# Kernel optimization log

Hardware: AMD Instinct MI355X
Metric: run time of the kernel (lower is better)

The kernel has to match this reference:

```python
import jax, jax.numpy as jnp
import numpy as np

N_NODES = 25000
N_EDGES = 400000
N_GRAPHS = 64
F_IN = 128


def setup_inputs() -> dict:
    key = jax.random.key(0)
    ks = jax.random.split(key, 16)
    inp = {}
    inp["x"] = jax.random.normal(ks[0], (N_NODES, F_IN), dtype=jnp.float32)
    inp["edge_index"] = jax.random.randint(ks[1], (2, N_EDGES), 0, N_NODES, dtype=jnp.int64)
    inp["edge_attr"] = jax.random.uniform(ks[2], (N_EDGES,), dtype=jnp.float32)
    inp["batch_ids"] = jnp.sort(jax.random.randint(ks[3], (N_NODES,), 0, N_GRAPHS, dtype=jnp.int64))
    def lin(k, fan_in, fan_out):
        bound = 1.0 / np.sqrt(fan_in)
        return jax.random.uniform(k, (fan_in, fan_out), dtype=jnp.float32, minval=-bound, maxval=bound)
    inp["W1_rel"] = lin(ks[4], F_IN, 512)
    inp["b1"] = jnp.zeros((512,), jnp.float32)
    inp["W1_root"] = lin(ks[5], F_IN, 512)
    inp["W2_rel"] = lin(ks[6], 512, 512)
    inp["b2"] = jnp.zeros((512,), jnp.float32)
    inp["W2_root"] = lin(ks[7], 512, 512)
    inp["Wl1"] = lin(ks[8], 512, 64)
    inp["bl1"] = jnp.zeros((64,), jnp.float32)
    inp["Wl2"] = lin(ks[9], 64, 16)
    inp["bl2"] = jnp.zeros((16,), jnp.float32)
    inp["Wl3"] = lin(ks[10], 16, 1)
    inp["bl3"] = jnp.zeros((1,), jnp.float32)
    return inp


def _graph_conv(h, src, dst, edge_attr, W_rel, b_rel, W_root, n_nodes):
    # PyG GraphConv: lin_rel(scatter_add(w_e * x_src, dst)) + lin_root(x)
    msg = h[src] * edge_attr[:, None]                       # [E, F] gather
    agg = jax.ops.segment_sum(msg, dst, num_segments=n_nodes)  # [N, F] scatter-add
    return agg @ W_rel + b_rel + h @ W_root


def reference(x, edge_index, edge_attr, batch_ids, W1_rel, b1, W1_root,
              W2_rel, b2, W2_root, Wl1, bl1, Wl2, bl2, Wl3, bl3):
    n_nodes = x.shape[0]
    src, dst = edge_index[0], edge_index[1]
    h = jax.nn.relu(_graph_conv(x, src, dst, edge_attr, W1_rel, b1, W1_root, n_nodes))
    h = jax.nn.relu(_graph_conv(h, src, dst, edge_attr, W2_rel, b2, W2_root, n_nodes))
    # global mean pool by graph id
    sums = jax.ops.segment_sum(h, batch_ids, num_segments=N_GRAPHS)  # [G, 512]
    counts = jax.ops.segment_sum(jnp.ones((n_nodes,), h.dtype), batch_ids, num_segments=N_GRAPHS)
    g = sums / jnp.maximum(counts, 1.0)[:, None]
    # dropout is identity in eval mode
    g = jax.nn.relu(g @ Wl1 + bl1)
    g = jax.nn.relu(g @ Wl2 + bl2)
    return g @ Wl3 + bl3  # [G, 1]
```

## Files before the change

kernel.cpp:

```cpp
#include <hip/hip_runtime.h>
#include <hip/hip_bf16.h>
#include <hip/hip_fp16.h>
#include <stdint.h>

#define N_NODESC 25000
#define N_EDGESC 400000
#define N_GRAPHSC 64
#define F_INC 128
#define HIDC 512
#define PSTRIDE 1600000
#define MTILES 196

typedef __attribute__((ext_vector_type(8))) short short8;
typedef __attribute__((ext_vector_type(8))) _Float16 half8;
typedef __attribute__((ext_vector_type(4))) float f32x4;

__device__ __forceinline__ unsigned short f2h(float f) {
  return __half_as_ushort(__float2half_rn(f));
}

__global__ __launch_bounds__(256)
void prep_kernel(const float* __restrict__ x, const int* __restrict__ ei,
                 const float* __restrict__ W1rel, const float* __restrict__ W1root,
                 const float* __restrict__ W2rel, const float* __restrict__ W2root,
                 unsigned short* __restrict__ xp, unsigned short* __restrict__ W1T,
                 unsigned short* __restrict__ W2T, int* __restrict__ deg,
                 float* __restrict__ gsum) {
  int blk = blockIdx.x, t = threadIdx.x;
  if (blk < 1563) {
    int e = blk * 256 + t;
    if (e < N_EDGESC) atomicAdd(&deg[ei[N_EDGESC + e]], 1);
  } else if (blk < 4688) {
    int idx = ((blk - 1563) * 256 + t) * 4;
    int node = idx >> 7;
    int col = idx & 127;
    float4 v = *(const float4*)(x + idx);
    ushort4 o;
    o.x = f2h(v.x); o.y = f2h(v.y); o.z = f2h(v.z); o.w = f2h(v.w);
    *(ushort4*)(xp + (size_t)(col >> 6) * PSTRIDE + (size_t)node * 64 + (col & 63)) = o;
  } else if (blk < 4848) {
    __shared__ float tile[64][65];
    int b2 = blk - 4688;
    const float* src;
    unsigned short* dst;
    int n0, k0, Kout;
    if (b2 < 128) {
      int kt = b2 >> 3, nt = b2 & 7;
      k0 = kt * 64; n0 = nt * 64;
      src = (k0 < 512) ? (W2rel + (size_t)k0 * 512) : (W2root + (size_t)(k0 - 512) * 512);
      dst = W2T; Kout = 1024;
    } else {
      int b = b2 - 128;
      int kt = b >> 3, nt = b & 7;
      k0 = kt * 64; n0 = nt * 64;
      src = (k0 < 128) ? (W1rel + (size_t)k0 * 512) : (W1root + (size_t)(k0 - 128) * 512);
      dst = W1T; Kout = 256;
    }
    int c = t & 63;
    int r4 = t >> 6;
#pragma unroll
    for (int rr = 0; rr < 64; rr += 4) {
      int row = rr + r4;
      tile[c][row] = src[(size_t)row * 512 + n0 + c];
    }
    __syncthreads();
#pragma unroll
    for (int rr = 0; rr < 64; rr += 4) {
      int nrow = rr + r4;
      dst[(size_t)(n0 + nrow) * Kout + k0 + c] = f2h(tile[nrow][c]);
    }
  } else {
    int i = (blk - 4848) * 256 + t;
    if (i < N_GRAPHSC * HIDC) gsum[i] = 0.f;
  }
}

__global__ __launch_bounds__(1024)
void scan_kernel(const int* __restrict__ deg, int* __restrict__ indptr, int* __restrict__ cursor,
                 int* __restrict__ sorted) {
  __shared__ int sums[1024];
  __shared__ int bins[256];
  __shared__ int binptr[256];
  const int t = threadIdx.x;
  const int CH = (N_NODESC + 1023) / 1024;
  const int base = t * CH;
  const unsigned ub = (unsigned)deg[N_NODESC];
  if (t < 256) bins[t] = 0;
  __syncthreads();
  int dl[CH];
  int s = 0;
  for (int i = 0; i < CH; ++i) {
    int idx = base + i;
    int d = (idx < N_NODESC) ? (int)((unsigned)deg[idx] - ub) : -1;
    dl[i] = d;
    if (d >= 0) {
      s += d;
      atomicAdd(&bins[d > 255 ? 255 : d], 1);
    }
  }
  sums[t] = s;
  __syncthreads();
  for (int off = 1; off < 1024; off <<= 1) {
    int v = (t >= off) ? sums[t - off] : 0;
    __syncthreads();
    sums[t] += v;
    __syncthreads();
  }
  if (t == 0) {
    int run = 0;
    for (int b = 0; b < 256; ++b) { binptr[b] = run; run += bins[b]; }
  }
  __syncthreads();
  int run = (t > 0) ? sums[t - 1] : 0;
  for (int i = 0; i < CH; ++i) {
    int idx = base + i;
    if (idx < N_NODESC) {
      indptr[idx] = run;
      cursor[idx] = run;
      run += dl[i];
      int pos = atomicAdd(&binptr[dl[i] > 255 ? 255 : dl[i]], 1);
      sorted[pos] = idx;
    }
  }
  if (t == 0) indptr[N_NODESC] = sums[1023];
}

__global__ void fill_kernel(const int* __restrict__ ei, const float* __restrict__ ea,
                            int* __restrict__ cursor, unsigned* __restrict__ emeta) {
  int e = blockIdx.x * blockDim.x + threadIdx.x;
  if (e >= N_EDGESC) return;
  int dst = ei[N_EDGESC + e];
  int pos = atomicAdd(&cursor[dst], 1);
  unsigned short hw = __half_as_ushort(__float2half_rn(ea[e]));
  emeta[pos] = (unsigned)ei[e] | ((unsigned)hw << 16);
}

__global__ __launch_bounds__(256)
void agg_gather_s(const unsigned short* __restrict__ feat, const int* __restrict__ indptr,
                  const unsigned* __restrict__ emeta, const int* __restrict__ sorted,
                  unsigned short* __restrict__ outp, int lgP) {
  int panel = blockIdx.x & ((1 << lgP) - 1);
  int nidx = (blockIdx.x >> lgP) * 32 + (threadIdx.x >> 3);
  if (nidx >= N_NODESC) return;
  int c8 = threadIdx.x & 7;
  int node = sorted[nidx];
  int beg = indptr[node];
  int deg = indptr[node + 1] - beg;
  const unsigned* mp = emeta + beg;
  const char* fb = (const char*)(feat + (size_t)panel * PSTRIDE);
  unsigned coff = c8 * 16u;
  float acc[8] = {};
  int j = 0;
  for (; j + 2 <= deg; j += 2) {
    unsigned mA = mp[j];
    unsigned mB = mp[j + 1];
    half8 vA = *(const half8*)(fb + (mA & 0xffffu) * 128u + coff);
    half8 vB = *(const half8*)(fb + (mB & 0xffffu) * 128u + coff);
    float wA = __half2float(__ushort_as_half((unsigned short)(mA >> 16)));
    float wB = __half2float(__ushort_as_half((unsigned short)(mB >> 16)));
#pragma unroll
    for (int c = 0; c < 8; ++c) acc[c] += (float)vA[c] * wA;
#pragma unroll
    for (int c = 0; c < 8; ++c) acc[c] += (float)vB[c] * wB;
  }
  if (j < deg) {
    unsigned mA = mp[j];
    half8 vA = *(const half8*)(fb + (mA & 0xffffu) * 128u + coff);
    float wA = __half2float(__ushort_as_half((unsigned short)(mA >> 16)));
#pragma unroll
    for (int c = 0; c < 8; ++c) acc[c] += (float)vA[c] * wA;
  }
  half8 o;
#pragma unroll
  for (int c = 0; c < 8; ++c) o[c] = (_Float16)acc[c];
  *(half8*)(outp + (size_t)panel * PSTRIDE + (size_t)node * 64 + c8 * 8) = o;
}

__device__ __forceinline__ void gemm_map(int b, int& m0, int& n0) {
  if (b < 768) {
    int u = b & 7;
    int v = b >> 3;
    m0 = ((v >> 2) * 8 + u) * 128;
    n0 = (v & 3) * 128;
  } else {
    int r = b - 768;
    m0 = (192 + (r >> 2)) * 128;
    n0 = (r & 3) * 128;
  }
}

__global__ __launch_bounds__(256, 3)
void gemm_bt_relu(const short* __restrict__ A0, const short* __restrict__ A1,
                  const short* __restrict__ BT, const float* __restrict__ bias,
                  unsigned short* __restrict__ Outp, int M, int S) {
  const int K = 2 * S;
  __shared__ __align__(16) short As[128 * 64];
  __shared__ __align__(16) short Bs[128 * 64];
  int m0, n0;
  gemm_map(blockIdx.x, m0, n0);
  const int tid = threadIdx.x;
  const int wave = tid >> 6;
  const int lane = tid & 63;
  const int quad = lane >> 4;
  const int r = lane & 15;
  const int wm = (wave >> 1) * 64;
  const int wn = (wave & 1) * 64;

  f32x4 acc[4][4] = {};

  const int nk = K >> 6;
  for (int kt = 0; kt < nk; ++kt) {
    const int kbase = kt << 6;
    const short* Ab;
    int koff;
    if (kbase < S) { Ab = A0; koff = kbase; } else { Ab = A1; koff = kbase - S; }
    const short* Apan = Ab + (size_t)(koff >> 6) * PSTRIDE;
#pragma unroll
    for (int i = 0; i < 4; ++i) {
      int s = ((wave * 4 + i) << 6) + lane;
      int row = s >> 3;
      int c = (s & 7) ^ (row & 7);
      int rg = m0 + row; if (rg > M - 1) rg = M - 1;
      const short* gp = Apan + (size_t)rg * 64 + (c << 3);
      __builtin_amdgcn_global_load_lds((const __attribute__((address_space(1))) void*)gp,
                                       (__attribute__((address_space(3))) void*)&As[(wave * 4 + i) * 512],
                                       16, 0, 0);
    }
#pragma unroll
    for (int i = 0; i < 4; ++i) {
      int s = ((wave * 4 + i) << 6) + lane;
      int row = s >> 3;
      int c = (s & 7) ^ (row & 7);
      const short* gp = BT + (size_t)(n0 + row) * K + kbase + (c << 3);
      __builtin_amdgcn_global_load_lds((const __attribute__((address_space(1))) void*)gp,
                                       (__attribute__((address_space(3))) void*)&Bs[(wave * 4 + i) * 512],
                                       16, 0, 0);
    }
    __syncthreads();
#pragma unroll
    for (int ks = 0; ks < 2; ++ks) {
      half8 af[4], bfr[4];
#pragma unroll
      for (int tm = 0; tm < 4; ++tm) {
        int ml = wm + tm * 16 + r;
        int c = (ks << 2) + quad;
        int slot = ml * 8 + (c ^ (ml & 7));
        af[tm] = *(const half8*)&As[slot * 8];
      }
#pragma unroll
      for (int tn = 0; tn < 4; ++tn) {
        int nl = wn + tn * 16 + r;
        int c = (ks << 2) + quad;
        int slot = nl * 8 + (c ^ (nl & 7));
        bfr[tn] = *(const half8*)&Bs[slot * 8];
      }
#pragma unroll
      for (int tm = 0; tm < 4; ++tm)
#pragma unroll
        for (int tn = 0; tn < 4; ++tn)
          acc[tm][tn] = __builtin_amdgcn_mfma_f32_16x16x32_f16(af[tm], bfr[tn], acc[tm][tn], 0, 0, 0);
    }
    __syncthreads();
  }

#pragma unroll
  for (int tm = 0; tm < 4; ++tm) {
    int rowb = m0 + wm + tm * 16 + quad * 4;
#pragma unroll
    for (int tn = 0; tn < 4; ++tn) {
      int col = n0 + wn + tn * 16 + r;
      float bv = bias[col];
      unsigned short* obase = Outp + (size_t)(col >> 6) * PSTRIDE + (col & 63);
#pragma unroll
      for (int reg = 0; reg < 4; ++reg) {
        int rr = rowb + reg;
        if (rr < M) {
          float v = acc[tm][tn][reg] + bv;
          v = v > 0.f ? v : 0.f;
          obase[(size_t)rr * 64] = f2h(v);
        }
      }
    }
  }
}

__global__ __launch_bounds__(256, 3)
void gemm_bt_pool(const short* __restrict__ A0, const short* __restrict__ A1,
                  const short* __restrict__ BT, const float* __restrict__ bias,
                  const int* __restrict__ batch, float* __restrict__ gsum, int M, int S) {
  const int K = 2 * S;
  __shared__ __align__(16) short As[128 * 64];
  __shared__ __align__(16) short Bs[128 * 64];
  int m0, n0;
  gemm_map(blockIdx.x, m0, n0);
  const int tid = threadIdx.x;
  const int wave = tid >> 6;
  const int lane = tid & 63;
  const int quad = lane >> 4;
  const int r = lane & 15;
  const int wm = (wave >> 1) * 64;
  const int wn = (wave & 1) * 64;

  f32x4 acc[4][4] = {};

  const int nk = K >> 6;
  for (int kt = 0; kt < nk; ++kt) {
    const int kbase = kt << 6;
    const short* Ab;
    int koff;
    if (kbase < S) { Ab = A0; koff = kbase; } else { Ab = A1; koff = kbase - S; }
    const short* Apan = Ab + (size_t)(koff >> 6) * PSTRIDE;
#pragma unroll
    for (int i = 0; i < 4; ++i) {
      int s = ((wave * 4 + i) << 6) + lane;
      int row = s >> 3;
      int c = (s & 7) ^ (row & 7);
      int rg = m0 + row; if (rg > M - 1) rg = M - 1;
      const short* gp = Apan + (size_t)rg * 64 + (c << 3);
      __builtin_amdgcn_global_load_lds((const __attribute__((address_space(1))) void*)gp,
                                       (__attribute__((address_space(3))) void*)&As[(wave * 4 + i) * 512],
                                       16, 0, 0);
    }
#pragma unroll
    for (int i = 0; i < 4; ++i) {
      int s = ((wave * 4 + i) << 6) + lane;
      int row = s >> 3;
      int c = (s & 7) ^ (row & 7);
      const short* gp = BT + (size_t)(n0 + row) * K + kbase + (c << 3);
      __builtin_amdgcn_global_load_lds((const __attribute__((address_space(1))) void*)gp,
                                       (__attribute__((address_space(3))) void*)&Bs[(wave * 4 + i) * 512],
                                       16, 0, 0);
    }
    __syncthreads();
#pragma unroll
    for (int ks = 0; ks < 2; ++ks) {
      half8 af[4], bfr[4];
#pragma unroll
      for (int tm = 0; tm < 4; ++tm) {
        int ml = wm + tm * 16 + r;
        int c = (ks << 2) + quad;
        int slot = ml * 8 + (c ^ (ml & 7));
        af[tm] = *(const half8*)&As[slot * 8];
      }
#pragma unroll
      for (int tn = 0; tn < 4; ++tn) {
        int nl = wn + tn * 16 + r;
        int c = (ks << 2) + quad;
        int slot = nl * 8 + (c ^ (nl & 7));
        bfr[tn] = *(const half8*)&Bs[slot * 8];
      }
#pragma unroll
      for (int tm = 0; tm < 4; ++tm)
#pragma unroll
        for (int tn = 0; tn < 4; ++tn)
          acc[tm][tn] = __builtin_amdgcn_mfma_f32_16x16x32_f16(af[tm], bfr[tn], acc[tm][tn], 0, 0, 0);
    }
    __syncthreads();
  }

  int gid[4][4];
#pragma unroll
  for (int tm = 0; tm < 4; ++tm) {
    int rowb = m0 + wm + tm * 16 + quad * 4;
#pragma unroll
    for (int reg = 0; reg < 4; ++reg) {
      int rr = rowb + reg;
      gid[tm][reg] = batch[rr < M ? rr : (M - 1)];
    }
#pragma unroll
    for (int tn = 0; tn < 4; ++tn) {
      float bv = bias[n0 + wn + tn * 16 + r];
#pragma unroll
      for (int reg = 0; reg < 4; ++reg) {
        int rr = rowb + reg;
        float v = acc[tm][tn][reg] + bv;
        v = v > 0.f ? v : 0.f;
        acc[tm][tn][reg] = (rr < M) ? v : 0.f;
      }
    }
  }
  int g_lo = batch[m0 < M ? m0 : (M - 1)];
  int g_hi = batch[(m0 + 127) < M ? (m0 + 127) : (M - 1)];
  for (int g = g_lo; g <= g_hi; ++g) {
#pragma unroll
    for (int tn = 0; tn < 4; ++tn) {
      float s = 0.f;
#pragma unroll
      for (int tm = 0; tm < 4; ++tm)
#pragma unroll
        for (int reg = 0; reg < 4; ++reg)
          s += (gid[tm][reg] == g) ? acc[tm][tn][reg] : 0.f;
      s += __shfl_xor(s, 16);
      s += __shfl_xor(s, 32);
      if (quad == 0)
        atomicAdd(&gsum[(size_t)g * HIDC + n0 + wn + tn * 16 + r], s);
    }
  }
}

__global__ __launch_bounds__(256)
void mlp_kernel(const float* __restrict__ gsum, const int* __restrict__ batch,
                const float* __restrict__ Wl1, const float* __restrict__ bl1,
                const float* __restrict__ Wl2, const float* __restrict__ bl2,
                const float* __restrict__ Wl3, const float* __restrict__ bl3,
                float* __restrict__ out) {
  int gi = blockIdx.x;
  int t = threadIdx.x;
  int unit = t & 63;
  int part = t >> 6;
  __shared__ float red[4][64];
  __shared__ float h1s[64];
  __shared__ float h2s[16];
  int lo = 0, hi = N_NODESC;
  while (lo < hi) { int mid = (lo + hi) >> 1; if (batch[mid] < gi) lo = mid + 1; else hi = mid; }
  int start = lo;
  hi = N_NODESC;
  while (lo < hi) { int mid = (lo + hi) >> 1; if (batch[mid] < gi + 1) lo = mid + 1; else hi = mid; }
  float inv = 1.0f / fmaxf((float)(lo - start), 1.0f);
  const float* gr = gsum + gi * HIDC;
  float acc = 0.f;
  for (int j = part * 128; j < (part + 1) * 128; ++j)
    acc += gr[j] * Wl1[j * 64 + unit];
  red[part][unit] = acc;
  __syncthreads();
  if (t < 64) {
    float a = bl1[t] + (red[0][t] + red[1][t] + red[2][t] + red[3][t]) * inv;
    h1s[t] = fmaxf(a, 0.f);
  }
  __syncthreads();
  if (t < 16) {
    float a = bl2[t];
    for (int j = 0; j < 64; ++j) a += h1s[j] * Wl2[j * 16 + t];
    h2s[t] = fmaxf(a, 0.f);
  }
  __syncthreads();
  if (t == 0) {
    float a = bl3[0];
    for (int j = 0; j < 16; ++j) a += h2s[j] * Wl3[j];
    out[gi] = a;
  }
}

extern "C" void kernel_launch(void* const* d_in, const int* in_sizes, int n_in,
                              void* d_out, int out_size, void* d_ws, size_t ws_size,
                              hipStream_t stream) {
  const float* x      = (const float*)d_in[0];
  const int*   ei     = (const int*)d_in[1];
  const float* ea     = (const float*)d_in[2];
  const int*   batch  = (const int*)d_in[3];
  const float* W1rel  = (const float*)d_in[4];
  const float* b1     = (const float*)d_in[5];
  const float* W1root = (const float*)d_in[6];
  const float* W2rel  = (const float*)d_in[7];
  const float* b2     = (const float*)d_in[8];
  const float* W2root = (const float*)d_in[9];
  const float* Wl1    = (const float*)d_in[10];
  const float* bl1    = (const float*)d_in[11];
  const float* Wl2    = (const float*)d_in[12];
  const float* bl2    = (const float*)d_in[13];
  const float* Wl3    = (const float*)d_in[14];
  const float* bl3    = (const float*)d_in[15];
  float* out = (float*)d_out;

  char* ws = (char*)d_ws;
  unsigned short* xp     = (unsigned short*)(ws + 0);
  unsigned short* agg1p  = (unsigned short*)(ws + 6400000);
  unsigned short* h1p    = (unsigned short*)(ws + 12800000);
  unsigned short* agg2p  = (unsigned short*)(ws + 38400000);
  unsigned short* W1T    = (unsigned short*)(ws + 64000000);
  unsigned short* W2T    = (unsigned short*)(ws + 64262144);
  float*          gsum   = (float*)(ws + 65310720);
  int*            deg    = (int*)(ws + 65441792);
  int*            cursor = (int*)(ws + 65541796);
  int*            indptr = (int*)(ws + 65641796);
  unsigned*       emeta  = (unsigned*)(ws + 65741812);
  int*            sorted = (int*)(ws + 67341812);

  prep_kernel<<<4976, 256, 0, stream>>>(x, ei, W1rel, W1root, W2rel, W2root,
                                        xp, W1T, W2T, deg, gsum);
  scan_kernel<<<1, 1024, 0, stream>>>(deg, indptr, cursor, sorted);
  fill_kernel<<<(N_EDGESC + 255) / 256, 256, 0, stream>>>(ei, ea, cursor, emeta);

  const int NBLK = (N_NODESC + 31) / 32;
  agg_gather_s<<<NBLK * 2, 256, 0, stream>>>(xp, indptr, emeta, sorted, agg1p, 1);

  gemm_bt_relu<<<784, 256, 0, stream>>>((const short*)agg1p, (const short*)xp,
                                        (const short*)W1T, b1, h1p, N_NODESC, 128);

  agg_gather_s<<<NBLK * 8, 256, 0, stream>>>(h1p, indptr, emeta, sorted, agg2p, 3);

  gemm_bt_pool<<<784, 256, 0, stream>>>((const short*)agg2p, (const short*)h1p,
                                        (const short*)W2T, b2, batch, gsum, N_NODESC, 512);

  mlp_kernel<<<N_GRAPHSC, 256, 0, stream>>>(gsum, batch, Wl1, bl1, Wl2, bl2, Wl3, bl3, out);
}
```

Baseline: 303.8 us.

## Restructure GEMMs into 128x256 tiles with triple-buffered LDS prefetch pipeline

Both GEMM kernels now share a core that uses 512-thread blocks computing 128x256 output tiles. LDS is triple-buffered and global-to-LDS loads for tile t+2 are issued during MFMA compute on tile t. The loop uses explicit vmcnt waits, raw s_barrier, s_setprio around MFMA bursts, and precomputed swizzled LDS offsets. Block mapping is also changed to an XCD-aware order. The aim is to hide load latency and reuse each A tile across more columns, at the cost of lower occupancy (one block per CU, large LDS footprint) and fragile hand-managed synchronization.

New measurement: 309.4 us. About the same (+1.9%).

```diff
diff --git a/kernel.cpp b/kernel.cpp
--- a/kernel.cpp
+++ b/kernel.cpp
@@ -9,7 +9,6 @@
 #define F_INC 128
 #define HIDC 512
 #define PSTRIDE 1600000
-#define MTILES 196
 
 typedef __attribute__((ext_vector_type(8))) short short8;
 typedef __attribute__((ext_vector_type(8))) _Float16 half8;
@@ -176,92 +175,163 @@
   *(half8*)(outp + (size_t)panel * PSTRIDE + (size_t)node * 64 + c8 * 8) = o;
 }
 
-__device__ __forceinline__ void gemm_map(int b, int& m0, int& n0) {
-  if (b < 768) {
-    int u = b & 7;
-    int v = b >> 3;
-    m0 = ((v >> 2) * 8 + u) * 128;
-    n0 = (v & 3) * 128;
-  } else {
-    int r = b - 768;
-    m0 = (192 + (r >> 2)) * 128;
-    n0 = (r & 3) * 128;
-  }
-}
-
-__global__ __launch_bounds__(256, 3)
-void gemm_bt_relu(const short* __restrict__ A0, const short* __restrict__ A1,
-                  const short* __restrict__ BT, const float* __restrict__ bias,
-                  unsigned short* __restrict__ Outp, int M, int S) {
+__device__ __forceinline__ void gemm_map2(int b, int& m0, int& n0) {
+  int g = (b & 7) * 49 + (b >> 3);
+  m0 = (g >> 1) << 7;
+  n0 = (g & 1) << 8;
+}
+
+__device__ __forceinline__ void stage_a(const short* Apan, int m0, int M,
+                                        short* dst, int wave, int lane) {
+#pragma unroll
+  for (int i = 0; i < 2; ++i) {
+    int s = ((i * 8 + wave) << 6) + lane;
+    int row = s >> 3;
+    int c = (s & 7) ^ (row & 7);
+    int rg = m0 + row;
+    if (rg > M - 1) rg = M - 1;
+    const short* gp = Apan + (size_t)rg * 64 + (c << 3);
+    __builtin_amdgcn_global_load_lds(
+        (const __attribute__((address_space(1))) void*)gp,
+        (__attribute__((address_space(3))) void*)(dst + ((i * 8 + wave) << 9)),
+        16, 0, 0);
+  }
+}
+
+template <int I0, int I1>
+__device__ __forceinline__ void stage_b(const short* BT, int n0, int K, int kbase,
+                                        short* dst, int wave, int lane) {
+#pragma unroll
+  for (int i = I0; i < I1; ++i) {
+    int s = ((i * 8 + wave) << 6) + lane;
+    int row = s >> 3;
+    int c = (s & 7) ^ (row & 7);
+    const short* gp = BT + (size_t)(n0 + row) * K + kbase + (c << 3);
+    __builtin_amdgcn_global_load_lds(
+        (const __attribute__((address_space(1))) void*)gp,
+        (__attribute__((address_space(3))) void*)(dst + ((i * 8 + wave) << 9)),
+        16, 0, 0);
+  }
+}
+
+__device__ __forceinline__ const short* apan_sel(const short* A0, const short* A1,
+                                                 int S, int kt) {
+  int kb = kt << 6;
+  const short* Ab = (kb < S) ? A0 : A1;
+  int koff = (kb < S) ? kb : kb - S;
+  return Ab + (size_t)(koff >> 6) * PSTRIDE;
+}
+
+__device__ __forceinline__ void wg_barrier() {
+  asm volatile("" ::: "memory");
+  __builtin_amdgcn_s_barrier();
+  asm volatile("" ::: "memory");
+}
+
+__device__ __forceinline__ void gemm_core(const short* A0, const short* A1,
+                                          const short* BT, int M, int S,
+                                          int m0, int n0, short* As, short* Bs,
+                                          f32x4 (&acc)[4][4]) {
   const int K = 2 * S;
-  __shared__ __align__(16) short As[128 * 64];
-  __shared__ __align__(16) short Bs[128 * 64];
-  int m0, n0;
-  gemm_map(blockIdx.x, m0, n0);
+  const int nk = K >> 6;
   const int tid = threadIdx.x;
   const int wave = tid >> 6;
   const int lane = tid & 63;
   const int quad = lane >> 4;
   const int r = lane & 15;
-  const int wm = (wave >> 1) * 64;
-  const int wn = (wave & 1) * 64;
+  const int wm = (wave >> 2) << 6;
+  const int wn = (wave & 3) << 6;
+
+  int aoff[2][4], boff[2][4];
+#pragma unroll
+  for (int p = 0; p < 2; ++p) {
+#pragma unroll
+    for (int tm = 0; tm < 4; ++tm) {
+      int ml = wm + tm * 16 + r;
+      int c = (p << 2) + quad;
+      aoff[p][tm] = (ml * 8 + (c ^ (ml & 7))) * 8;
+    }
+#pragma unroll
+    for (int tn = 0; tn < 4; ++tn) {
+      int nl = wn + tn * 16 + r;
+      int c = (p << 2) + quad;
+      boff[p][tn] = (nl * 8 + (c ^ (nl & 7))) * 8;
+    }
+  }
+
+  stage_a(apan_sel(A0, A1, S, 0), m0, M, As, wave, lane);
+  stage_b<0, 4>(BT, n0, K, 0, Bs, wave, lane);
+  stage_a(apan_sel(A0, A1, S, 1), m0, M, As + 8192, wave, lane);
+  stage_b<0, 4>(BT, n0, K, 64, Bs + 16384, wave, lane);
+  asm volatile("s_waitcnt vmcnt(6)");
+  wg_barrier();
+
+  int cur = 0, nxt = 2;
+  for (int t = 0; t < nk; ++t) {
+    int kt2 = (t + 2 < nk) ? t + 2 : nk - 1;
+    const short* Ap2 = apan_sel(A0, A1, S, kt2);
+    int kb2 = kt2 << 6;
+    short* Ad = As + nxt * 8192;
+    short* Bd = Bs + nxt * 16384;
+    const short* Ac = As + cur * 8192;
+    const short* Bc = Bs + cur * 16384;
+
+    half8 af[4], bf[4];
+#pragma unroll
+    for (int tm = 0; tm < 4; ++tm) af[tm] = *(const half8*)&Ac[aoff[0][tm]];
+#pragma unroll
+    for (int tn = 0; tn < 4; ++tn) bf[tn] = *(const half8*)&Bc[boff[0][tn]];
+    stage_a(Ap2, m0, M, Ad, wave, lane);
+    stage_b<0, 1>(BT, n0, K, kb2, Bd, wave, lane);
+    wg_barrier();
+    __builtin_amdgcn_s_setprio(1);
+#pragma unroll
+    for (int tm = 0; tm < 4; ++tm)
+#pragma unroll
+      for (int tn = 0; tn < 4; ++tn)
+        acc[tm][tn] = __builtin_amdgcn_mfma_f32_16x16x32_f16(af[tm], bf[tn], acc[tm][tn], 0, 0, 0);
+    __builtin_amdgcn_s_setprio(0);
+    wg_barrier();
+
+#pragma unroll
+    for (int tm = 0; tm < 4; ++tm) af[tm] = *(const half8*)&Ac[aoff[1][tm]];
+#pragma unroll
+    for (int tn = 0; tn < 4; ++tn) bf[tn] = *(const half8*)&Bc[boff[1][tn]];
+    stage_b<1, 4>(BT, n0, K, kb2, Bd, wave, lane);
+    wg_barrier();
+    __builtin_amdgcn_s_setprio(1);
+#pragma unroll
+    for (int tm = 0; tm < 4; ++tm)
+#pragma unroll
+      for (int tn = 0; tn < 4; ++tn)
+        acc[tm][tn] = __builtin_amdgcn_mfma_f32_16x16x32_f16(af[tm], bf[tn], acc[tm][tn], 0, 0, 0);
+    __builtin_amdgcn_s_setprio(0);
+    asm volatile("s_waitcnt vmcnt(6)");
+    wg_barrier();
+
+    cur = (cur == 2) ? 0 : cur + 1;
+    nxt = (nxt == 2) ? 0 : nxt + 1;
+  }
+  asm volatile("s_waitcnt vmcnt(0)");
+}
+
+__global__ __launch_bounds__(512, 1)
+void gemm_bt_relu(const short* __restrict__ A0, const short* __restrict__ A1,
+                  const short* __restrict__ BT, const float* __restrict__ bias,
+                  unsigned short* __restrict__ Outp, int M, int S) {
+  __shared__ __align__(16) short As[3 * 8192];
+  __shared__ __align__(16) short Bs[3 * 16384];
+  int m0, n0;
+  gemm_map2(blockIdx.x, m0, n0);
+  const int wave = threadIdx.x >> 6;
+  const int lane = threadIdx.x & 63;
+  const int quad = lane >> 4;
+  const int r = lane & 15;
+  const int wm = (wave >> 2) << 6;
+  const int wn = (wave & 3) << 6;
 
   f32x4 acc[4][4] = {};
-
-  const int nk = K >> 6;
-  for (int kt = 0; kt < nk; ++kt) {
-    const int kbase = kt << 6;
-    const short* Ab;
-    int koff;
-    if (kbase < S) { Ab = A0; koff = kbase; } else { Ab = A1; koff = kbase - S; }
-    const short* Apan = Ab + (size_t)(koff >> 6) * PSTRIDE;
-#pragma unroll
-    for (int i = 0; i < 4; ++i) {
-      int s = ((wave * 4 + i) << 6) + lane;
-      int row = s >> 3;
-      int c = (s & 7) ^ (row & 7);
-      int rg = m0 + row; if (rg > M - 1) rg = M - 1;
-      const short* gp = Apan + (size_t)rg * 64 + (c << 3);
-      __builtin_amdgcn_global_load_lds((const __attribute__((address_space(1))) void*)gp,
-                                       (__attribute__((address_space(3))) void*)&As[(wave * 4 + i) * 512],
-                                       16, 0, 0);
-    }
-#pragma unroll
-    for (int i = 0; i < 4; ++i) {
-      int s = ((wave * 4 + i) << 6) + lane;
-      int row = s >> 3;
-      int c = (s & 7) ^ (row & 7);
-      const short* gp = BT + (size_t)(n0 + row) * K + kbase + (c << 3);
-      __builtin_amdgcn_global_load_lds((const __attribute__((address_space(1))) void*)gp,
-                                       (__attribute__((address_space(3))) void*)&Bs[(wave * 4 + i) * 512],
-                                       16, 0, 0);
-    }
-    __syncthreads();
-#pragma unroll
-    for (int ks = 0; ks < 2; ++ks) {
-      half8 af[4], bfr[4];
-#pragma unroll
-      for (int tm = 0; tm < 4; ++tm) {
-        int ml = wm + tm * 16 + r;
-        int c = (ks << 2) + quad;
-        int slot = ml * 8 + (c ^ (ml & 7));
-        af[tm] = *(const half8*)&As[slot * 8];
-      }
-#pragma unroll
-      for (int tn = 0; tn < 4; ++tn) {
-        int nl = wn + tn * 16 + r;
-        int c = (ks << 2) + quad;
-        int slot = nl * 8 + (c ^ (nl & 7));
-        bfr[tn] = *(const half8*)&Bs[slot * 8];
-      }
-#pragma unroll
-      for (int tm = 0; tm < 4; ++tm)
-#pragma unroll
-        for (int tn = 0; tn < 4; ++tn)
-          acc[tm][tn] = __builtin_amdgcn_mfma_f32_16x16x32_f16(af[tm], bfr[tn], acc[tm][tn], 0, 0, 0);
-    }
-    __syncthreads();
-  }
+  gemm_core(A0, A1, BT, M, S, m0, n0, As, Bs, acc);
 
 #pragma unroll
   for (int tm = 0; tm < 4; ++tm) {
@@ -284,79 +354,23 @@
   }
 }
 
-__global__ __launch_bounds__(256, 3)
+__global__ __launch_bounds__(512, 1)
 void gemm_bt_pool(const short* __restrict__ A0, const short* __restrict__ A1,
                   const short* __restrict__ BT, const float* __restrict__ bias,
                   const int* __restrict__ batch, float* __restrict__ gsum, int M, int S) {
-  const int K = 2 * S;
-  __shared__ __align__(16) short As[128 * 64];
-  __shared__ __align__(16) short Bs[128 * 64];
+  __shared__ __align__(16) short As[3 * 8192];
+  __shared__ __align__(16) short Bs[3 * 16384];
   int m0, n0;
-  gemm_map(blockIdx.x, m0, n0);
-  const int tid = threadIdx.x;
-  const int wave = tid >> 6;
-  const int lane = tid & 63;
+  gemm_map2(blockIdx.x, m0, n0);
+  const int wave = threadIdx.x >> 6;
+  const int lane = threadIdx.x & 63;
   const int quad = lane >> 4;
   const int r = lane & 15;
-  const int wm = (wave >> 1) * 64;
-  const int wn = (wave & 1) * 64;
+  const int wm = (wave >> 2) << 6;
+  const int wn = (wave & 3) << 6;
 
   f32x4 acc[4][4] = {};
-
-  const int nk = K >> 6;
-  for (int kt = 0; kt < nk; ++kt) {
-    const int kbase = kt << 6;
-    const short* Ab;
-    int koff;
-    if (kbase < S) { Ab = A0; koff = kbase; } else { Ab = A1; koff = kbase - S; }
-    const short* Apan = Ab + (size_t)(koff >> 6) * PSTRIDE;
-#pragma unroll
-    for (int i = 0; i < 4; ++i) {
-      int s = ((wave * 4 + i) << 6) + lane;
-      int row = s >> 3;
-      int c = (s & 7) ^ (row & 7);
-      int rg = m0 + row; if (rg > M - 1) rg = M - 1;
-      const short* gp = Apan + (size_t)rg * 64 + (c << 3);
-      __builtin_amdgcn_global_load_lds((const __attribute__((address_space(1))) void*)gp,
-                                       (__attribute__((address_space(3))) void*)&As[(wave * 4 + i) * 512],
-                                       16, 0, 0);
-    }
-#pragma unroll
-    for (int i = 0; i < 4; ++i) {
-      int s = ((wave * 4 + i) << 6) + lane;
-      int row = s >> 3;
-      int c = (s & 7) ^ (row & 7);
-      const short* gp = BT + (size_t)(n0 + row) * K + kbase + (c << 3);
-      __builtin_amdgcn_global_load_lds((const __attribute__((address_space(1))) void*)gp,
-                                       (__attribute__((address_space(3))) void*)&Bs[(wave * 4 + i) * 512],
-                                       16, 0, 0);
-    }
-    __syncthreads();
-#pragma unroll
-    for (int ks = 0; ks < 2; ++ks) {
-      half8 af[4], bfr[4];
-#pragma unroll
-      for (int tm = 0; tm < 4; ++tm) {
-        int ml = wm + tm * 16 + r;
-        int c = (ks << 2) + quad;
-        int slot = ml * 8 + (c ^ (ml & 7));
-        af[tm] = *(const half8*)&As[slot * 8];
-      }
-#pragma unroll
-      for (int tn = 0; tn < 4; ++tn) {
-        int nl = wn + tn * 16 + r;
-        int c = (ks << 2) + quad;
-        int slot = nl * 8 + (c ^ (nl & 7));
-        bfr[tn] = *(const half8*)&Bs[slot * 8];
-      }
-#pragma unroll
-      for (int tm = 0; tm < 4; ++tm)
-#pragma unroll
-        for (int tn = 0; tn < 4; ++tn)
-          acc[tm][tn] = __builtin_amdgcn_mfma_f32_16x16x32_f16(af[tm], bfr[tn], acc[tm][tn], 0, 0, 0);
-    }
-    __syncthreads();
-  }
+  gemm_core(A0, A1, BT, M, S, m0, n0, As, Bs, acc);
 
   int gid[4][4];
 #pragma unroll
@@ -484,12 +498,12 @@
   const int NBLK = (N_NODESC + 31) / 32;
   agg_gather_s<<<NBLK * 2, 256, 0, stream>>>(xp, indptr, emeta, sorted, agg1p, 1);
 
-  gemm_bt_relu<<<784, 256, 0, stream>>>((const short*)agg1p, (const short*)xp,
+  gemm_bt_relu<<<392, 512, 0, stream>>>((const short*)agg1p, (const short*)xp,
                                         (const short*)W1T, b1, h1p, N_NODESC, 128);
 
   agg_gather_s<<<NBLK * 8, 256, 0, stream>>>(h1p, indptr, emeta, sorted, agg2p, 3);
 
-  gemm_bt_pool<<<784, 256, 0, stream>>>((const short*)agg2p, (const short*)h1p,
+  gemm_bt_pool<<<392, 512, 0, stream>>>((const short*)agg2p, (const short*)h1p,
                                         (const short*)W2T, b2, batch, gsum, N_NODESC, 512);
 
   mlp_kernel<<<N_GRAPHSC, 256, 0, stream>>>(gsum, batch, Wl1, bl1, Wl2, bl2, Wl3, bl3, out);
```
